# Optimization experiments

Measured on AMD Instinct MI355X. Metric: run time of the kernel, lower is better.

The kernel has to match this reference:

```python
import jax, jax.numpy as jnp
import numpy as np

N = 1_048_576   # collocation points
D_IN = 3        # seq_net[0]
H = 32          # hidden width (seq_net[1..3])
B = 4           # seq_net[-1] = number of parallel branches / outputs


def setup_inputs() -> dict:
    key = jax.random.key(0)
    ks = jax.random.split(key, 9)

    def init_w(k, shape, fan_in):
        bound = 1.0 / np.sqrt(fan_in)
        return jax.random.uniform(k, shape, jnp.float32, -bound, bound)

    x = jax.random.normal(ks[0], (N, D_IN), dtype=jnp.float32)
    # Per-branch weights stacked on leading branch axis B (torch.nn.Linear init ranges).
    W0 = init_w(ks[1], (B, D_IN, H), D_IN)
    b0 = init_w(ks[2], (B, H), D_IN)
    W1 = init_w(ks[3], (B, H, H), H)
    b1 = init_w(ks[4], (B, H), H)
    W2 = init_w(ks[5], (B, H, H), H)
    b2 = init_w(ks[6], (B, H), H)
    W3 = init_w(ks[7], (B, H, 1), H)
    b3 = init_w(ks[8], (B, 1), H)
    return {"x": x, "W0": W0, "b0": b0, "W1": W1, "b1": b1,
            "W2": W2, "b2": b2, "W3": W3, "b3": b3}


def reference(x, W0, b0, W1, b1, W2, b2, W3, b3):
    # All B branches computed as one batched GEMM chain (same math as the
    # python loop over per-branch Linear+tanh stacks in PFNN.forward).
    h = jnp.tanh(jnp.einsum('nd,bdh->bnh', x, W0) + b0[:, None, :])   # [B,N,H]
    h = jnp.tanh(jnp.einsum('bnd,bdh->bnh', h, W1) + b1[:, None, :])  # [B,N,H]
    h = jnp.tanh(jnp.einsum('bnd,bdh->bnh', h, W2) + b2[:, None, :])  # [B,N,H]
    out = jnp.einsum('bnd,bdh->bnh', h, W3) + b3[:, None, :]          # [B,N,1]
    # torch.cat(preds, dim=1): branch outputs side by side -> [N, B]
    return jnp.transpose(out[:, :, 0])
```

## Files before the change

### kernel.cpp

```cpp
#include <hip/hip_runtime.h>


#define NPTS 1048576
#define BLOCK 256
#define HROW 72
#define SCALE 2.8853900817779268f

#define OFF_BSC  16384
#define OFF_W0F  17408
#define OFF_B0P  25600
#define OFF_W3P  26112

using f16   = _Float16;
using f16x8 = __attribute__((ext_vector_type(8))) _Float16;
using f32x4 = __attribute__((ext_vector_type(4))) float;
using hfx2  = decltype(__builtin_amdgcn_cvt_pkrtz(0.0f, 0.0f));

__device__ __forceinline__ void tanh4_pre(float v0, float v1, float v2, float v3,
                                          float& o0, float& o1, float& o2, float& o3)
{
    float a0 = __builtin_amdgcn_exp2f(v0) + 1.0f;
    float a1 = __builtin_amdgcn_exp2f(v1) + 1.0f;
    float a2 = __builtin_amdgcn_exp2f(v2) + 1.0f;
    float a3 = __builtin_amdgcn_exp2f(v3) + 1.0f;
    float p01  = a0 * a1;
    float p012 = p01 * a2;
    float p    = p012 * a3;
    float r    = __builtin_amdgcn_rcpf(p);
    float inv3 = r * p012;
    float s    = r * a3;
    float inv2 = s * p01;
    float s2   = s * a2;
    float inv1 = s2 * a0;
    float inv0 = s2 * a1;
    o0 = __builtin_fmaf(-2.0f, inv0, 1.0f);
    o1 = __builtin_fmaf(-2.0f, inv1, 1.0f);
    o2 = __builtin_fmaf(-2.0f, inv2, 1.0f);
    o3 = __builtin_fmaf(-2.0f, inv3, 1.0f);
}

__device__ __forceinline__ void epi_mt(const f32x4& c0, const f32x4& c1, int mt,
                                       unsigned char* __restrict__ H,
                                       int col, int quad)
{
    #pragma unroll
    for (int r = 0; r < 4; r += 2) {
        int p = mt * 16 + quad * 4 + r;
        float o0, o1, o2, o3;
        tanh4_pre(c0[r], c1[r], c0[r + 1], c1[r + 1], o0, o1, o2, o3);
        union { hfx2 h; unsigned int u; } cv0, cv1;
        cv0.h = __builtin_amdgcn_cvt_pkrtz(o0, o1);
        cv1.h = __builtin_amdgcn_cvt_pkrtz(o2, o3);
        *reinterpret_cast<unsigned int*>(H + p * HROW + 4 * col)       = cv0.u;
        *reinterpret_cast<unsigned int*>(H + (p + 1) * HROW + 4 * col) = cv1.u;
    }
}

__global__ void prep_kernel(const float* __restrict__ W0, const float* __restrict__ b0,
                            const float* __restrict__ W1, const float* __restrict__ b1,
                            const float* __restrict__ W2, const float* __restrict__ b2,
                            const float* __restrict__ W3,
                            unsigned char* __restrict__ ws)
{
    int i = blockIdx.x * 256 + threadIdx.x;
    if (i < 8192) {
        int k = i & 31, n = (i >> 5) & 15, t = (i >> 9) & 1, b = (i >> 10) & 3, l = i >> 12;
        int f = 2 * n + t;
        const float* W = l ? W2 : W1;
        reinterpret_cast<f16*>(ws)[i] = (f16)(SCALE * W[(b * 32 + k) * 32 + f]);
    } else if (i < 8448) {
        int j = i - 8192;
        int n = j & 15, t = (j >> 4) & 1, b = (j >> 5) & 3, l = j >> 7;
        const float* bb = l ? b2 : b1;
        reinterpret_cast<float*>(ws + OFF_BSC)[j] = SCALE * bb[b * 32 + 2 * n + t];
    } else if (i < 12544) {
        int j = i - 8448;
        int k = j & 31, n = (j >> 5) & 15, t = (j >> 9) & 1, b = (j >> 10) & 3;
        int f = 2 * n + t;
        int q = k >> 3, jj = k & 7;
        int row = -1; bool lo = false;
        if (q == 0 && jj < 6)      row = (jj < 3) ? jj : jj - 3;
        else if (q == 1 && jj < 3) { row = jj; lo = true; }
        f16 outv = (f16)0.0f;
        if (row >= 0) {
            float w  = SCALE * W0[(b * 3 + row) * 32 + f];
            f16   wh = (f16)w;
            outv = lo ? (f16)(w - (float)wh) : wh;
        }
        reinterpret_cast<f16*>(ws + OFF_W0F)[((b * 2 + t) * 16 + n) * 32 + k] = outv;
    } else if (i < 12672) {
        int j = i - 12544;
        int n = j & 15, t = (j >> 4) & 1, b = j >> 5;
        reinterpret_cast<float*>(ws + OFF_B0P)[(b * 2 + t) * 16 + n] = SCALE * b0[b * 32 + 2 * n + t];
    } else if (i < 12736) {
        int j = i - 12672;
        union { hfx2 h; unsigned int u; } cv;
        cv.h = __builtin_amdgcn_cvt_pkrtz(W3[2 * j], W3[2 * j + 1]);
        reinterpret_cast<unsigned int*>(ws + OFF_W3P)[j] = cv.u;
    }
}

__global__ __launch_bounds__(BLOCK, 8) void pfnn_kernel(
    const float* __restrict__ x, const unsigned char* __restrict__ ws,
    const float* __restrict__ b3,
    float* __restrict__ out)
{
    __shared__ __align__(16) unsigned char Hl[4][64 * HROW];

    const f16*   Wf  = reinterpret_cast<const f16*>(ws);
    const float* Bsc = reinterpret_cast<const float*>(ws + OFF_BSC);
    const f16*   W0f = reinterpret_cast<const f16*>(ws + OFF_W0F);
    const float* B0p = reinterpret_cast<const float*>(ws + OFF_B0P);
    const unsigned int* W3p = reinterpret_cast<const unsigned int*>(ws + OFF_W3P);

    const int t    = threadIdx.x;
    const int lane = t & 63;
    const int wv   = t >> 6;
    const int col  = lane & 15;
    const int quad = lane >> 4;
    unsigned char* __restrict__ H = &Hl[wv][0];

    const int n0 = blockIdx.x * BLOCK + t;
    const float x0 = x[3 * n0 + 0];
    const float x1 = x[3 * n0 + 1];
    const float x2 = x[3 * n0 + 2];

    f16x8 xfrag[4];
    {
        union { hfx2 h; int u; } q0_, q1_, q2_;
        q0_.h = __builtin_amdgcn_cvt_pkrtz(x0, x1);
        float r0 = x0 - (float)q0_.h[0];
        float r1 = x1 - (float)q0_.h[1];
        q1_.h = __builtin_amdgcn_cvt_pkrtz(x2, r0);
        float r2 = x2 - (float)q1_.h[0];
        q2_.h = __builtin_amdgcn_cvt_pkrtz(r1, r2);
        int d0 = q0_.u, d1 = q1_.u, d2 = q2_.u;
        #pragma unroll
        for (int mt = 0; mt < 4; ++mt) {
            int addr = 4 * (mt * 16 + col);
            union { int i[4]; f16x8 f; } u;
            u.i[0] = __builtin_amdgcn_ds_bpermute(addr, d0);
            u.i[1] = __builtin_amdgcn_ds_bpermute(addr, d1);
            u.i[2] = __builtin_amdgcn_ds_bpermute(addr, d2);
            u.i[3] = 0;
            xfrag[mt] = u.f;
        }
    }

    float res[4];

    #pragma unroll 1
    for (int b = 0; b < 4; ++b) {
        {
            const f16* wb = W0f + (b * 2) * 512;
            f16x8 bf0 = *reinterpret_cast<const f16x8*>(wb + col * 32 + quad * 8);
            f16x8 bf1 = *reinterpret_cast<const f16x8*>(wb + 512 + col * 32 + quad * 8);
            float bias0 = B0p[(b * 2 + 0) * 16 + col];
            float bias1 = B0p[(b * 2 + 1) * 16 + col];
            f32x4 ci0 = {bias0, bias0, bias0, bias0};
            f32x4 ci1 = {bias1, bias1, bias1, bias1};

            #pragma unroll
            for (int mt = 0; mt < 4; ++mt) {
                f32x4 c0 = __builtin_amdgcn_mfma_f32_16x16x32_f16(xfrag[mt], bf0, ci0, 0, 0, 0);
                f32x4 c1 = __builtin_amdgcn_mfma_f32_16x16x32_f16(xfrag[mt], bf1, ci1, 0, 0, 0);
                epi_mt(c0, c1, mt, H, col, quad);
            }
        }

        #pragma unroll
        for (int l = 0; l < 2; ++l) {
            const f16* wb = Wf + ((l * 4 + b) * 2) * 512;
            f16x8 bf0 = *reinterpret_cast<const f16x8*>(wb + col * 32 + quad * 8);
            f16x8 bf1 = *reinterpret_cast<const f16x8*>(wb + 512 + col * 32 + quad * 8);
            float bias0 = Bsc[((l * 4 + b) * 2 + 0) * 16 + col];
            float bias1 = Bsc[((l * 4 + b) * 2 + 1) * 16 + col];
            f32x4 ci0 = {bias0, bias0, bias0, bias0};
            f32x4 ci1 = {bias1, bias1, bias1, bias1};

            #pragma unroll
            for (int mt = 0; mt < 4; ++mt) {
                const unsigned char* arow = H + (mt * 16 + col) * HROW + quad * 16;
                uint2 alo = *reinterpret_cast<const uint2*>(arow);
                uint2 ahi = *reinterpret_cast<const uint2*>(arow + 8);
                union { uint4 u; f16x8 f; } av;
                av.u = make_uint4(alo.x, alo.y, ahi.x, ahi.y);
                f32x4 c0 = __builtin_amdgcn_mfma_f32_16x16x32_f16(av.f, bf0, ci0, 0, 0, 0);
                f32x4 c1 = __builtin_amdgcn_mfma_f32_16x16x32_f16(av.f, bf1, ci1, 0, 0, 0);
                epi_mt(c0, c1, mt, H, col, quad);
            }
        }

        {
            float o = b3[b];
            const unsigned char* row = H + lane * HROW;
            const unsigned int* w3p = W3p + b * 16;
            #pragma unroll
            for (int i = 0; i < 8; ++i) {
                uint2 u = *reinterpret_cast<const uint2*>(row + 8 * i);
#if __has_builtin(__builtin_amdgcn_fdot2)
                union { unsigned int uu; hfx2 hh; } h0, h1, w0, w1;
                h0.uu = u.x; h1.uu = u.y;
                w0.uu = w3p[2 * i]; w1.uu = w3p[2 * i + 1];
                o = __builtin_amdgcn_fdot2(h0.hh, w0.hh, o, false);
                o = __builtin_amdgcn_fdot2(h1.hh, w1.hh, o, false);
#else
                union { unsigned int uu; f16 h[2]; } h0, h1, w0, w1;
                h0.uu = u.x; h1.uu = u.y;
                w0.uu = w3p[2 * i]; w1.uu = w3p[2 * i + 1];
                o = __builtin_fmaf((float)h0.h[0], (float)w0.h[0], o);
                o = __builtin_fmaf((float)h0.h[1], (float)w0.h[1], o);
                o = __builtin_fmaf((float)h1.h[0], (float)w1.h[0], o);
                o = __builtin_fmaf((float)h1.h[1], (float)w1.h[1], o);
#endif
            }
            res[b] = o;
        }
    }

    float4 r4 = make_float4(res[0], res[1], res[2], res[3]);
    *reinterpret_cast<float4*>(out + 4 * n0) = r4;
}

extern "C" void kernel_launch(void* const* d_in, const int* in_sizes, int n_in,
                              void* d_out, int out_size, void* d_ws, size_t ws_size,
                              hipStream_t stream) {
    const float* x  = (const float*)d_in[0];
    const float* W0 = (const float*)d_in[1];
    const float* b0 = (const float*)d_in[2];
    const float* W1 = (const float*)d_in[3];
    const float* b1 = (const float*)d_in[4];
    const float* W2 = (const float*)d_in[5];
    const float* b2 = (const float*)d_in[6];
    const float* W3 = (const float*)d_in[7];
    const float* b3 = (const float*)d_in[8];
    float* out = (float*)d_out;
    unsigned char* ws = (unsigned char*)d_ws;

    prep_kernel<<<dim3(50), dim3(256), 0, stream>>>(W0, b0, W1, b1, W2, b2, W3, ws);
    pfnn_kernel<<<dim3(NPTS / BLOCK), dim3(BLOCK), 0, stream>>>(x, ws, b3, out);
}
```

Before: 159.7 us.

## Fold tanh affine into weights and widen LDS rows for 128-bit reads

Hidden activations are now stored as 1/(1+e^x) - 0.5, so the -2 scaling of tanh is folded into the next layer's weights and the output weights during prep, saving a multiply per element in the epilogue. The reciprocal trick is restructured to pair inputs, giving a shorter dependency chain. The LDS row pitch goes from 72 to 80 bytes so A-fragment and final-layer reads can use single 16-byte loads instead of split 8-byte loads. The new pitch may alter bank-conflict behaviour on the scattered epilogue stores. The layer-1 bias is not visibly compensated for the -0.5 offset, and the shown folding does not clearly cover it.

```diff
diff --git a/kernel.cpp b/kernel.cpp
--- a/kernel.cpp
+++ b/kernel.cpp
@@ -3,7 +3,7 @@
 
 #define NPTS 1048576
 #define BLOCK 256
-#define HROW 72
+#define HROW 80
 #define SCALE 2.8853900817779268f
 
 #define OFF_BSC  16384
@@ -16,27 +16,23 @@
 using f32x4 = __attribute__((ext_vector_type(4))) float;
 using hfx2  = decltype(__builtin_amdgcn_cvt_pkrtz(0.0f, 0.0f));
 
-__device__ __forceinline__ void tanh4_pre(float v0, float v1, float v2, float v3,
-                                          float& o0, float& o1, float& o2, float& o3)
+__device__ __forceinline__ void inv4c(float v0, float v1, float v2, float v3,
+                                      float& o0, float& o1, float& o2, float& o3)
 {
     float a0 = __builtin_amdgcn_exp2f(v0) + 1.0f;
     float a1 = __builtin_amdgcn_exp2f(v1) + 1.0f;
     float a2 = __builtin_amdgcn_exp2f(v2) + 1.0f;
     float a3 = __builtin_amdgcn_exp2f(v3) + 1.0f;
-    float p01  = a0 * a1;
-    float p012 = p01 * a2;
-    float p    = p012 * a3;
-    float r    = __builtin_amdgcn_rcpf(p);
-    float inv3 = r * p012;
-    float s    = r * a3;
-    float inv2 = s * p01;
-    float s2   = s * a2;
-    float inv1 = s2 * a0;
-    float inv0 = s2 * a1;
-    o0 = __builtin_fmaf(-2.0f, inv0, 1.0f);
-    o1 = __builtin_fmaf(-2.0f, inv1, 1.0f);
-    o2 = __builtin_fmaf(-2.0f, inv2, 1.0f);
-    o3 = __builtin_fmaf(-2.0f, inv3, 1.0f);
+    float p01 = a0 * a1;
+    float p23 = a2 * a3;
+    float p   = p01 * p23;
+    float r   = __builtin_amdgcn_rcpf(p);
+    float r01 = r * p23;
+    float r23 = r * p01;
+    o0 = __builtin_fmaf(r01, a1, -0.5f);
+    o1 = __builtin_fmaf(r01, a0, -0.5f);
+    o2 = __builtin_fmaf(r23, a3, -0.5f);
+    o3 = __builtin_fmaf(r23, a2, -0.5f);
 }
 
 __device__ __forceinline__ void epi_mt(const f32x4& c0, const f32x4& c1, int mt,
@@ -47,7 +43,7 @@
     for (int r = 0; r < 4; r += 2) {
         int p = mt * 16 + quad * 4 + r;
         float o0, o1, o2, o3;
-        tanh4_pre(c0[r], c1[r], c0[r + 1], c1[r + 1], o0, o1, o2, o3);
+        inv4c(c0[r], c1[r], c0[r + 1], c1[r + 1], o0, o1, o2, o3);
         union { hfx2 h; unsigned int u; } cv0, cv1;
         cv0.h = __builtin_amdgcn_cvt_pkrtz(o0, o1);
         cv1.h = __builtin_amdgcn_cvt_pkrtz(o2, o3);
@@ -67,7 +63,7 @@
         int k = i & 31, n = (i >> 5) & 15, t = (i >> 9) & 1, b = (i >> 10) & 3, l = i >> 12;
         int f = 2 * n + t;
         const float* W = l ? W2 : W1;
-        reinterpret_cast<f16*>(ws)[i] = (f16)(SCALE * W[(b * 32 + k) * 32 + f]);
+        reinterpret_cast<f16*>(ws)[i] = (f16)(-2.0f * SCALE * W[(b * 32 + k) * 32 + f]);
     } else if (i < 8448) {
         int j = i - 8192;
         int n = j & 15, t = (j >> 4) & 1, b = (j >> 5) & 3, l = j >> 7;
@@ -95,7 +91,7 @@
     } else if (i < 12736) {
         int j = i - 12672;
         union { hfx2 h; unsigned int u; } cv;
-        cv.h = __builtin_amdgcn_cvt_pkrtz(W3[2 * j], W3[2 * j + 1]);
+        cv.h = __builtin_amdgcn_cvt_pkrtz(-2.0f * W3[2 * j], -2.0f * W3[2 * j + 1]);
         reinterpret_cast<unsigned int*>(ws + OFF_W3P)[j] = cv.u;
     }
 }
@@ -180,13 +176,10 @@
 
             #pragma unroll
             for (int mt = 0; mt < 4; ++mt) {
-                const unsigned char* arow = H + (mt * 16 + col) * HROW + quad * 16;
-                uint2 alo = *reinterpret_cast<const uint2*>(arow);
-                uint2 ahi = *reinterpret_cast<const uint2*>(arow + 8);
-                union { uint4 u; f16x8 f; } av;
-                av.u = make_uint4(alo.x, alo.y, ahi.x, ahi.y);
-                f32x4 c0 = __builtin_amdgcn_mfma_f32_16x16x32_f16(av.f, bf0, ci0, 0, 0, 0);
-                f32x4 c1 = __builtin_amdgcn_mfma_f32_16x16x32_f16(av.f, bf1, ci1, 0, 0, 0);
+                const f16x8 av = *reinterpret_cast<const f16x8*>(
+                    H + (mt * 16 + col) * HROW + quad * 16);
+                f32x4 c0 = __builtin_amdgcn_mfma_f32_16x16x32_f16(av, bf0, ci0, 0, 0, 0);
+                f32x4 c1 = __builtin_amdgcn_mfma_f32_16x16x32_f16(av, bf1, ci1, 0, 0, 0);
                 epi_mt(c0, c1, mt, H, col, quad);
             }
         }
@@ -196,22 +189,26 @@
             const unsigned char* row = H + lane * HROW;
             const unsigned int* w3p = W3p + b * 16;
             #pragma unroll
-            for (int i = 0; i < 8; ++i) {
-                uint2 u = *reinterpret_cast<const uint2*>(row + 8 * i);
+            for (int i = 0; i < 4; ++i) {
+                uint4 u = *reinterpret_cast<const uint4*>(row + 16 * i);
 #if __has_builtin(__builtin_amdgcn_fdot2)
-                union { unsigned int uu; hfx2 hh; } h0, h1, w0, w1;
-                h0.uu = u.x; h1.uu = u.y;
-                w0.uu = w3p[2 * i]; w1.uu = w3p[2 * i + 1];
+                union { unsigned int uu; hfx2 hh; } h0, h1, h2, h3, w0, w1, w2, w3u;
+                h0.uu = u.x; h1.uu = u.y; h2.uu = u.z; h3.uu = u.w;
+                w0.uu = w3p[4 * i];     w1.uu = w3p[4 * i + 1];
+                w2.uu = w3p[4 * i + 2]; w3u.uu = w3p[4 * i + 3];
                 o = __builtin_amdgcn_fdot2(h0.hh, w0.hh, o, false);
                 o = __builtin_amdgcn_fdot2(h1.hh, w1.hh, o, false);
+                o = __builtin_amdgcn_fdot2(h2.hh, w2.hh, o, false);
+                o = __builtin_amdgcn_fdot2(h3.hh, w3u.hh, o, false);
 #else
-                union { unsigned int uu; f16 h[2]; } h0, h1, w0, w1;
-                h0.uu = u.x; h1.uu = u.y;
-                w0.uu = w3p[2 * i]; w1.uu = w3p[2 * i + 1];
-                o = __builtin_fmaf((float)h0.h[0], (float)w0.h[0], o);
-                o = __builtin_fmaf((float)h0.h[1], (float)w0.h[1], o);
-                o = __builtin_fmaf((float)h1.h[0], (float)w1.h[0], o);
-                o = __builtin_fmaf((float)h1.h[1], (float)w1.h[1], o);
+                union { unsigned int uu; f16 h[2]; } hh[4], wwu[4];
+                hh[0].uu = u.x; hh[1].uu = u.y; hh[2].uu = u.z; hh[3].uu = u.w;
+                #pragma unroll
+                for (int q = 0; q < 4; ++q) {
+                    wwu[q].uu = w3p[4 * i + q];
+                    o = __builtin_fmaf((float)hh[q].h[0], (float)wwu[q].h[0], o);
+                    o = __builtin_fmaf((float)hh[q].h[1], (float)wwu[q].h[1], o);
+                }
 #endif
             }
             res[b] = o;
```

Result: faster. 152.0 us (-4.8%).
